# Optimization experiments

Hardware: AMD Instinct MI355X
Metric: run time of the kernel (lower is better)

## Reference

```python
import jax, jax.numpy as jnp
import numpy as np
import math

B, H, T, N = 2, 16, 4096, 64  # N = mlp_internal_dim_multiplier * n_embd // n_head = 1*1024//16
THETA = 2.0 ** 16


def _cos_sin(T, N):
    # quantized-theta RoPE tables, matching get_freqs + angle construction
    t = jnp.arange(N, dtype=jnp.float32)
    tq = jnp.floor(t / 2.0) * 2.0                      # quantize(t, q=2)
    freqs = 1.0 / (THETA ** (tq / N)) / (2.0 * math.pi)  # [N]
    phases = jnp.arange(T, dtype=jnp.float32)[:, None] * freqs[None, :]  # [T,N]
    ang = (phases % 1.0) * (2.0 * math.pi)
    return jnp.cos(ang), jnp.sin(ang)                  # each [T,N]


def setup_inputs() -> dict:
    key = jax.random.key(0)
    kq, kv = jax.random.split(key)
    Q = jax.random.normal(kq, (B, H, T, N), dtype=jnp.float32)
    V = jax.random.normal(kv, (B, H, T, N), dtype=jnp.float32)
    return {"Q": Q, "V": V}


def reference(Q, V):
    # K is Q (asserted in the torch module); RoPE applied to Q only.
    b, h, t, n = Q.shape
    cos, sin = _cos_sin(t, n)                          # [t,n], broadcast over b,h
    q_rot = jnp.stack((-Q[..., 1::2], Q[..., ::2]), axis=-1).reshape(Q.shape)
    QR = Q * cos + q_rot * sin                         # [b,h,t,n]
    scores = jnp.einsum('bhtn,bhsn->bhts', QR, QR) * (n ** -0.5)
    # strict lower-triangular mask (tril with diagonal=-1): no softmax
    mask = jnp.tril(jnp.ones((t, t), dtype=bool), k=-1)
    scores = jnp.where(mask, scores, 0.0)
    return jnp.einsum('bhts,bhsn->bhtn', scores, V)
```

## Files before the change

kernel.cpp:

```cpp
#include <hip/hip_runtime.h>

#define T_SEQ 4096
#define NDIM 64
#define BH 32
#define TN (T_SEQ * NDIM)

typedef short short8 __attribute__((ext_vector_type(8)));
typedef float f32x16 __attribute__((ext_vector_type(16)));
typedef unsigned uint2e __attribute__((ext_vector_type(2)));

static __device__ __forceinline__ unsigned packbf(float lo, float hi) {
    unsigned r;
    asm("v_cvt_pk_bf16_f32 %0, %1, %2" : "=v"(r) : "v"(lo), "v"(hi));
    return r;
}
static __device__ __forceinline__ f32x16 mfma32(short8 a, short8 b, f32x16 c) {
    return __builtin_amdgcn_mfma_f32_32x32x16_bf16(a, b, c, 0, 0, 0);
}

static __device__ __forceinline__ void half_swap(unsigned &x, unsigned &y) {
#if __has_builtin(__builtin_amdgcn_permlane32_swap)
    uint2e r = __builtin_amdgcn_permlane32_swap(x, y, false, false);
    x = r[0]; y = r[1];
#else
    int sl = (((int)threadIdx.x & 63) ^ 32) << 2;
    unsigned bx = (unsigned)__builtin_amdgcn_ds_bpermute(sl, (int)x);
    unsigned by = (unsigned)__builtin_amdgcn_ds_bpermute(sl, (int)y);
    bool hi = (threadIdx.x & 32) != 0;
    unsigned nx = hi ? by : x;
    unsigned ny = hi ? y : bx;
    x = nx; y = ny;
#endif
}

static __device__ __forceinline__ void tile_to_frags(const f32x16 &sc, short8 &f0, short8 &f1) {
    unsigned d[4][2];
#pragma unroll
    for (int g = 0; g < 4; ++g) {
        d[g][0] = packbf(sc[4 * g + 0], sc[4 * g + 1]);
        d[g][1] = packbf(sc[4 * g + 2], sc[4 * g + 3]);
    }
    half_swap(d[0][0], d[1][0]);
    half_swap(d[0][1], d[1][1]);
    half_swap(d[2][0], d[3][0]);
    half_swap(d[2][1], d[3][1]);
    union { unsigned u[4]; short8 s; } a, b;
    a.u[0] = d[0][0]; a.u[1] = d[0][1]; a.u[2] = d[1][0]; a.u[3] = d[1][1];
    b.u[0] = d[2][0]; b.u[1] = d[2][1]; b.u[2] = d[3][0]; b.u[3] = d[3][1];
    f0 = a.s; f1 = b.s;
}

__global__ __launch_bounds__(256) void rope_kernel(const float* __restrict__ Q,
                                                   unsigned short* __restrict__ qf) {
    const int bhtb = blockIdx.x;
    const int tb = bhtb & 127;
    const int bh = bhtb >> 7;
    const int np = threadIdx.x & 31;
    const int tg = threadIdx.x >> 5;
    const float freq = exp2f(-0.5f * (float)np) * 0.15915494309189535f;
    const int kc = np >> 3, hi = (np >> 2) & 1, jw = np & 3;
    const float2* qsrc = (const float2*)(Q + ((size_t)bh * T_SEQ + tb * 32) * NDIM);
    unsigned* qdst = (unsigned*)(qf + (size_t)bh * TN + (size_t)tb * 32 * NDIM);
#pragma unroll
    for (int it = 0; it < 4; ++it) {
        const int tl = tg * 4 + it;
        const int t = tb * 32 + tl;
        float2 q = qsrc[tl * 32 + np];
        float ph = (float)t * freq;
        float ang = (ph - floorf(ph)) * 6.283185307179586f;
        float s, c;
        __sincosf(ang, &s, &c);
        float r0 = q.x * c - q.y * s;
        float r1 = q.y * c + q.x * s;
        qdst[kc * 256 + (tl * 2 + hi) * 4 + jw] = packbf(r0, r1);
    }
}

__global__ __launch_bounds__(256) void vtrans_kernel(const float* __restrict__ V,
                                                     unsigned short* __restrict__ vfr) {
    __shared__ float tile[128 * 65];
    const int sb = blockIdx.x;
    const int bh = blockIdx.y;
    const int tid = threadIdx.x;
    const float* vsrc = V + ((size_t)bh * T_SEQ + sb * 128) * NDIM;
#pragma unroll
    for (int i = 0; i < 8; ++i) {
        int e = (i * 256 + tid) * 4;
        int row = e >> 6, col = e & 63;
        float4 d4 = *(const float4*)(vsrc + e);
        tile[row * 65 + col + 0] = d4.x; tile[row * 65 + col + 1] = d4.y;
        tile[row * 65 + col + 2] = d4.z; tile[row * 65 + col + 3] = d4.w;
    }
    __syncthreads();
    unsigned short* dst = vfr + (size_t)bh * TN + (size_t)sb * 8192;
#pragma unroll
    for (int u = 0; u < 4; ++u) {
        int g = u * 256 + tid;
        int kc = g >> 7, dh = g & 127;
        int d = dh >> 1, hh = dh & 1;
        int sbase = kc * 16 + hh * 8;
        uint4 o;
        o.x = packbf(tile[(sbase + 0) * 65 + d] * 0.125f, tile[(sbase + 1) * 65 + d] * 0.125f);
        o.y = packbf(tile[(sbase + 2) * 65 + d] * 0.125f, tile[(sbase + 3) * 65 + d] * 0.125f);
        o.z = packbf(tile[(sbase + 4) * 65 + d] * 0.125f, tile[(sbase + 5) * 65 + d] * 0.125f);
        o.w = packbf(tile[(sbase + 6) * 65 + d] * 0.125f, tile[(sbase + 7) * 65 + d] * 0.125f);
        *(uint4*)(dst + g * 8) = o;
    }
}

static __device__ __forceinline__ void load_ak4(const unsigned short* qfh, int sb, int ws,
                                                int lhx16, short8 (&A)[2][4]) {
    const int r32base = sb * 4 + 2 * ws;
#pragma unroll
    for (int st2 = 0; st2 < 2; ++st2)
#pragma unroll
        for (int kc = 0; kc < 4; ++kc)
            A[st2][kc] = *(const short8*)(qfh + (size_t)((r32base + st2) * 4 + kc) * 512 + lhx16);
}
static __device__ __forceinline__ void load_vf8(const unsigned short* vfh, int sb, int ws,
                                                int lhx16, short8 (&V)[4][2]) {
#pragma unroll
    for (int kc4 = 0; kc4 < 4; ++kc4) {
        const size_t base = (size_t)sb * 8192 + (size_t)(4 * ws + kc4) * 1024 + lhx16;
        V[kc4][0] = *(const short8*)(vfh + base);
        V[kc4][1] = *(const short8*)(vfh + base + 512);
    }
}
static __device__ __forceinline__ void s_phase(const short8 (&ak)[2][4], const short8 (&bq)[2][4],
                                               const f32x16 &zc, f32x16 (&sacc)[2][2]) {
#pragma unroll
    for (int st2 = 0; st2 < 2; ++st2)
#pragma unroll
        for (int tt2 = 0; tt2 < 2; ++tt2) {
            f32x16 acc = mfma32(ak[st2][0], bq[tt2][0], zc);
            acc = mfma32(ak[st2][1], bq[tt2][1], acc);
            acc = mfma32(ak[st2][2], bq[tt2][2], acc);
            sacc[st2][tt2] = mfma32(ak[st2][3], bq[tt2][3], acc);
        }
}
static __device__ __forceinline__ void transform_all(const f32x16 (&sacc)[2][2], short8 (&pa)[2][4]) {
#pragma unroll
    for (int st2 = 0; st2 < 2; ++st2)
#pragma unroll
        for (int tt2 = 0; tt2 < 2; ++tt2)
            tile_to_frags(sacc[st2][tt2], pa[tt2][2 * st2 + 0], pa[tt2][2 * st2 + 1]);
}
static __device__ __forceinline__ void o_phase(const short8 (&pa)[2][4], const short8 (&vf)[4][2],
                                               f32x16 (&oacc)[2][2]) {
#pragma unroll
    for (int kc4 = 0; kc4 < 4; ++kc4) {
        oacc[0][0] = mfma32(pa[0][kc4], vf[kc4][0], oacc[0][0]);
        oacc[0][1] = mfma32(pa[0][kc4], vf[kc4][1], oacc[0][1]);
        oacc[1][0] = mfma32(pa[1][kc4], vf[kc4][0], oacc[1][0]);
        oacc[1][1] = mfma32(pa[1][kc4], vf[kc4][1], oacc[1][1]);
    }
}

__global__ __launch_bounds__(256, 2) void attn_kernel(const unsigned short* __restrict__ qf,
                                                      const unsigned short* __restrict__ vfr,
                                                      float* __restrict__ out) {
    __shared__ float4 red[2][4][4][64];

    const int tid = threadIdx.x;
    const int lane = tid & 63;
    const int w = tid >> 6;
    const int ws = w >> 1, wt = w & 1;
    const int l31 = lane & 31, hi = lane >> 5;

    const int blk = blockIdx.x;
    const int bh = blk & 31;
    const int qb = 31 - (blk >> 5);
    const int t0 = qb * 128;

    const unsigned short* qfh = qf + (size_t)bh * TN;
    const unsigned short* vfh = vfr + (size_t)bh * TN;
    float* out_h = out + (size_t)bh * TN;

    const int lhx16 = (l31 * 2 + hi) * 8;

    short8 bq[2][4];
#pragma unroll
    for (int tt2 = 0; tt2 < 2; ++tt2) {
        const int r32 = (t0 >> 5) + 2 * wt + tt2;
#pragma unroll
        for (int kc = 0; kc < 4; ++kc)
            bq[tt2][kc] = *(const short8*)(qfh + (size_t)(r32 * 4 + kc) * 512 + lhx16);
    }

    f32x16 zc;
#pragma unroll
    for (int r = 0; r < 16; ++r) zc[r] = 0.0f;

    f32x16 oacc[2][2];
#pragma unroll
    for (int a = 0; a < 2; ++a)
#pragma unroll
        for (int b = 0; b < 2; ++b)
#pragma unroll
            for (int r = 0; r < 16; ++r) oacc[a][b][r] = 0.0f;

    short8 ak[2][4], vf[4][2];
    f32x16 sacc[2][2];
    load_ak4(qfh, 0, ws, lhx16, ak);
    load_vf8(vfh, 0, ws, lhx16, vf);
    s_phase(ak, bq, zc, sacc);
    load_ak4(qfh, (1 <= qb ? 1 : qb), ws, lhx16, ak);

    for (int sb = 0; sb < qb; ++sb) {
        short8 pa[2][4];
        transform_all(sacc, pa);
        o_phase(pa, vf, oacc);
        load_vf8(vfh, sb + 1, ws, lhx16, vf);
        s_phase(ak, bq, zc, sacc);
        const int nak = (sb + 2 <= qb) ? sb + 2 : qb;
        load_ak4(qfh, nak, ws, lhx16, ak);
    }

    {
#pragma unroll
        for (int st2 = 0; st2 < 2; ++st2) {
            const int st = 2 * ws + st2;
#pragma unroll
            for (int tt2 = 0; tt2 < 2; ++tt2) {
                const int tg = (2 * wt + tt2) * 32 + l31;
#pragma unroll
                for (int r = 0; r < 16; ++r) {
                    const int sg = st * 32 + (r & 3) + 8 * (r >> 2) + 4 * hi;
                    if (sg >= tg) sacc[st2][tt2][r] = 0.0f;
                }
            }
        }
        short8 pa[2][4];
        transform_all(sacc, pa);
        o_phase(pa, vf, oacc);
    }

    if (ws == 1) {
#pragma unroll
        for (int tt2 = 0; tt2 < 2; ++tt2)
#pragma unroll
            for (int dd = 0; dd < 2; ++dd)
#pragma unroll
                for (int g = 0; g < 4; ++g) {
                    float4 v;
                    v.x = oacc[tt2][dd][4 * g + 0];
                    v.y = oacc[tt2][dd][4 * g + 1];
                    v.z = oacc[tt2][dd][4 * g + 2];
                    v.w = oacc[tt2][dd][4 * g + 3];
                    red[wt][tt2 * 2 + dd][g][lane] = v;
                }
    }
    __syncthreads();
    if (ws == 0) {
#pragma unroll
        for (int tt2 = 0; tt2 < 2; ++tt2)
#pragma unroll
            for (int dd = 0; dd < 2; ++dd) {
#pragma unroll
                for (int g = 0; g < 4; ++g) {
                    float4 o = red[wt][tt2 * 2 + dd][g][lane];
                    oacc[tt2][dd][4 * g + 0] += o.x;
                    oacc[tt2][dd][4 * g + 1] += o.y;
                    oacc[tt2][dd][4 * g + 2] += o.z;
                    oacc[tt2][dd][4 * g + 3] += o.w;
                }
#pragma unroll
                for (int r = 0; r < 16; ++r) {
                    const int rl = (r & 3) + 8 * (r >> 2) + 4 * hi;
                    out_h[(size_t)(t0 + 64 * wt + 32 * tt2 + rl) * NDIM + 32 * dd + l31] =
                        oacc[tt2][dd][r];
                }
            }
    }
}

extern "C" void kernel_launch(void* const* d_in, const int* in_sizes, int n_in,
                              void* d_out, int out_size, void* d_ws, size_t ws_size,
                              hipStream_t stream) {
    (void)in_sizes; (void)n_in; (void)out_size; (void)ws_size;
    const float* Q = (const float*)d_in[0];
    const float* V = (const float*)d_in[1];
    float* out = (float*)d_out;

    unsigned short* qf  = (unsigned short*)d_ws;
    unsigned short* vfr = qf + (size_t)BH * TN;

    rope_kernel<<<BH * 128, 256, 0, stream>>>(Q, qf);
    vtrans_kernel<<<dim3(T_SEQ / 128, BH), 256, 0, stream>>>(V, vfr);
    attn_kernel<<<BH * 32, 256, 0, stream>>>(qf, vfr, out);
}
```

Baseline: 169.3 us.

## Interleave S and O MFMA halves with VALU transforms and sched_group_barrier pipelining

Splits the per-block S computation, score-to-fragment transform and O accumulation into halves. They are interleaved so the VALU conversion of one half overlaps the MFMAs of the other. The V loads for the next block are moved after the S phase, and sched_group_barrier hints interleave VALU, MFMA and global-load groups inside the loop. This is meant to hide the VALU conversion and load latency behind matrix work. It risks higher register pressure at 2 waves/SIMD and a compiler schedule that does not match the barrier counts.

```diff
diff --git a/kernel.cpp b/kernel.cpp
--- a/kernel.cpp
+++ b/kernel.cpp
@@ -126,34 +126,40 @@
         V[kc4][1] = *(const short8*)(vfh + base + 512);
     }
 }
-static __device__ __forceinline__ void s_phase(const short8 (&ak)[2][4], const short8 (&bq)[2][4],
-                                               const f32x16 &zc, f32x16 (&sacc)[2][2]) {
-#pragma unroll
-    for (int st2 = 0; st2 < 2; ++st2)
-#pragma unroll
-        for (int tt2 = 0; tt2 < 2; ++tt2) {
-            f32x16 acc = mfma32(ak[st2][0], bq[tt2][0], zc);
-            acc = mfma32(ak[st2][1], bq[tt2][1], acc);
-            acc = mfma32(ak[st2][2], bq[tt2][2], acc);
-            sacc[st2][tt2] = mfma32(ak[st2][3], bq[tt2][3], acc);
-        }
-}
-static __device__ __forceinline__ void transform_all(const f32x16 (&sacc)[2][2], short8 (&pa)[2][4]) {
-#pragma unroll
-    for (int st2 = 0; st2 < 2; ++st2)
-#pragma unroll
-        for (int tt2 = 0; tt2 < 2; ++tt2)
-            tile_to_frags(sacc[st2][tt2], pa[tt2][2 * st2 + 0], pa[tt2][2 * st2 + 1]);
-}
-static __device__ __forceinline__ void o_phase(const short8 (&pa)[2][4], const short8 (&vf)[4][2],
-                                               f32x16 (&oacc)[2][2]) {
-#pragma unroll
-    for (int kc4 = 0; kc4 < 4; ++kc4) {
+static __device__ __forceinline__ void t_half(int h, const f32x16 (&sacc)[2][2], short8 (&pa)[2][4]) {
+#pragma unroll
+    for (int tt2 = 0; tt2 < 2; ++tt2)
+        tile_to_frags(sacc[h][tt2], pa[tt2][2 * h + 0], pa[tt2][2 * h + 1]);
+}
+static __device__ __forceinline__ void s_half(int h, const short8 (&ak)[2][4], const short8 (&bq)[2][4],
+                                              const f32x16 &zc, f32x16 (&sacc)[2][2]) {
+#pragma unroll
+    for (int tt2 = 0; tt2 < 2; ++tt2) {
+        f32x16 acc = mfma32(ak[h][0], bq[tt2][0], zc);
+        acc = mfma32(ak[h][1], bq[tt2][1], acc);
+        acc = mfma32(ak[h][2], bq[tt2][2], acc);
+        sacc[h][tt2] = mfma32(ak[h][3], bq[tt2][3], acc);
+    }
+}
+static __device__ __forceinline__ void o_half(int h, const short8 (&pa)[2][4], const short8 (&vf)[4][2],
+                                              f32x16 (&oacc)[2][2]) {
+#pragma unroll
+    for (int i = 0; i < 2; ++i) {
+        const int kc4 = 2 * h + i;
         oacc[0][0] = mfma32(pa[0][kc4], vf[kc4][0], oacc[0][0]);
         oacc[0][1] = mfma32(pa[0][kc4], vf[kc4][1], oacc[0][1]);
         oacc[1][0] = mfma32(pa[1][kc4], vf[kc4][0], oacc[1][0]);
         oacc[1][1] = mfma32(pa[1][kc4], vf[kc4][1], oacc[1][1]);
     }
+}
+static __device__ __forceinline__ void o_phase(const short8 (&pa)[2][4], const short8 (&vf)[4][2],
+                                               f32x16 (&oacc)[2][2]) {
+    o_half(0, pa, vf, oacc);
+    o_half(1, pa, vf, oacc);
+}
+static __device__ __forceinline__ void transform_all(const f32x16 (&sacc)[2][2], short8 (&pa)[2][4]) {
+    t_half(0, sacc, pa);
+    t_half(1, sacc, pa);
 }
 
 __global__ __launch_bounds__(256, 2) void attn_kernel(const unsigned short* __restrict__ qf,
@@ -203,17 +209,27 @@
     f32x16 sacc[2][2];
     load_ak4(qfh, 0, ws, lhx16, ak);
     load_vf8(vfh, 0, ws, lhx16, vf);
-    s_phase(ak, bq, zc, sacc);
+    s_half(0, ak, bq, zc, sacc);
+    s_half(1, ak, bq, zc, sacc);
     load_ak4(qfh, (1 <= qb ? 1 : qb), ws, lhx16, ak);
 
     for (int sb = 0; sb < qb; ++sb) {
         short8 pa[2][4];
-        transform_all(sacc, pa);
-        o_phase(pa, vf, oacc);
-        load_vf8(vfh, sb + 1, ws, lhx16, vf);
-        s_phase(ak, bq, zc, sacc);
+        t_half(0, sacc, pa);
+        s_half(0, ak, bq, zc, sacc);
+        t_half(1, sacc, pa);
+        o_half(0, pa, vf, oacc);
+        s_half(1, ak, bq, zc, sacc);
+        o_half(1, pa, vf, oacc);
         const int nak = (sb + 2 <= qb) ? sb + 2 : qb;
         load_ak4(qfh, nak, ws, lhx16, ak);
+        load_vf8(vfh, sb + 1, ws, lhx16, vf);
+#pragma unroll
+        for (int g = 0; g < 8; ++g) {
+            __builtin_amdgcn_sched_group_barrier(0x002, 7, 0);
+            __builtin_amdgcn_sched_group_barrier(0x008, 4, 0);
+            __builtin_amdgcn_sched_group_barrier(0x020, 2, 0);
+        }
     }
 
     {
```

After: 177.5 us. 4.8% more time.
